# Performance work log

Hardware: AMD Instinct MI355X
Metric: run time of the kernel (lower is better)

## Reference

```python
import jax, jax.numpy as jnp
import numpy as np

NUM_STEPS = 3
NUM_HEADS = 8
HEAD_DIM = 128
EPS = 1e-5


def layernorm(x, g, b):
    mu = jnp.mean(x, -1, keepdims=True)
    var = jnp.mean(jnp.square(x - mu), -1, keepdims=True)
    return (x - mu) * jax.lax.rsqrt(var + EPS) * g + b


def entmax15(x):
    # Exact entmax-1.5 along last axis (Peters & Martins 2019, sort-based).
    x = (x - jnp.max(x, -1, keepdims=True)) / 2.0
    xs = jnp.flip(jnp.sort(x, -1), -1)  # descending sort
    rho = jnp.arange(1, x.shape[-1] + 1, dtype=x.dtype)
    mean = jnp.cumsum(xs, -1) / rho
    meansq = jnp.cumsum(xs * xs, -1) / rho
    ss = rho * (meansq - jnp.square(mean))
    tau = mean - jnp.sqrt(jnp.clip((1.0 - ss) / rho, 0.0, None))
    support = jnp.sum(tau <= xs, -1, keepdims=True)
    tau_star = jnp.take_along_axis(tau, support - 1, -1)
    return jnp.square(jnp.clip(x - tau_star, 0.0, None))


def setup_inputs() -> dict:
    key = jax.random.key(0)
    ks = jax.random.split(key, 6)
    B, S, Hd, Md, N = 2, 1024, 2048, 1024, 2048
    THD = NUM_HEADS * HEAD_DIM
    return {
        "hidden": jax.random.normal(ks[0], (B, S, Hd), jnp.float32),
        "memory": jax.random.normal(ks[1], (N, Md), jnp.float32),
        "Wq": jax.random.normal(ks[2], (THD, Hd), jnp.float32) / np.float32(np.sqrt(Hd)),
        "Wk": jax.random.normal(ks[3], (THD, Md), jnp.float32) / np.float32(np.sqrt(Md)),
        "Wv": jax.random.normal(ks[4], (THD, Md), jnp.float32) / np.float32(np.sqrt(Md)),
        "Wo": jax.random.normal(ks[5], (Hd, THD), jnp.float32) / np.float32(np.sqrt(THD)),
        "log_beta": jnp.full((NUM_HEADS,), float(np.log(1.0 / np.sqrt(HEAD_DIM))), jnp.float32),
        "g_state": jnp.ones((Hd,), jnp.float32),
        "b_state": jnp.zeros((Hd,), jnp.float32),
        "g_mem": jnp.ones((Md,), jnp.float32),
        "b_mem": jnp.zeros((Md,), jnp.float32),
    }


def reference(hidden, memory, Wq, Wk, Wv, Wo, log_beta, g_state, b_state, g_mem, b_mem):
    B, S, _ = hidden.shape
    N = memory.shape[0]
    H, hd = NUM_HEADS, HEAD_DIM
    # projections
    Q = layernorm(hidden, g_state, b_state) @ Wq.T            # (B,S,H*hd)
    mn = layernorm(memory, g_mem, b_mem)                      # (N,Md)
    K = (mn @ Wk.T).reshape(N, H, hd).transpose(1, 0, 2)      # (H,N,hd)
    V = (mn @ Wv.T).reshape(N, H, hd).transpose(1, 0, 2)      # (H,N,hd)
    xi = Q.reshape(B, S, H, hd).transpose(0, 2, 1, 3)          # (B,H,S,hd)
    beta = jnp.exp(log_beta)[None, :, None, None]
    for _ in range(NUM_STEPS):
        scores = jnp.einsum('bhsd,hnd->bhsn', xi, K) * beta    # (B,H,S,N)
        w = entmax15(scores)
        xi = jnp.einsum('bhsn,hnd->bhsd', w, V)
    out = xi.transpose(0, 2, 1, 3).reshape(B, S, H * hd) @ Wo.T  # (B,S,hidden_dim)
    return out
```

## Files before the change

kernel.cpp:

```cpp
#include <hip/hip_runtime.h>

typedef _Float16 half8 __attribute__((ext_vector_type(8)));
typedef _Float16 hv4 __attribute__((ext_vector_type(4)));
typedef float fv4 __attribute__((ext_vector_type(4)));

typedef __attribute__((address_space(3))) unsigned lds_u32;
typedef const __attribute__((address_space(1))) unsigned glb_u32;

__device__ __forceinline__ void gll16(const void* g, void* l) {
  __builtin_amdgcn_global_load_lds((glb_u32*)g, (lds_u32*)l, 16, 0, 0);
}

__global__ __launch_bounds__(256) void ln_rows(const float* __restrict__ in,
                                               const float* __restrict__ g,
                                               const float* __restrict__ bb,
                                               _Float16* __restrict__ out, int ncols) {
  __shared__ float sm[8];
  int row = blockIdx.x, t = threadIdx.x;
  const float* rp = in + (size_t)row * ncols;
  int nv = ncols >> 10;
  fv4 v[2];
  float s1 = 0.f, s2 = 0.f;
#pragma unroll
  for (int c = 0; c < 2; ++c)
    if (c < nv) {
      v[c] = *(const fv4*)(rp + c * 1024 + t * 4);
#pragma unroll
      for (int j = 0; j < 4; ++j) { s1 += v[c][j]; s2 += v[c][j] * v[c][j]; }
    }
#pragma unroll
  for (int off = 32; off > 0; off >>= 1) { s1 += __shfl_xor(s1, off, 64); s2 += __shfl_xor(s2, off, 64); }
  int w = t >> 6;
  if ((t & 63) == 0) { sm[w] = s1; sm[4 + w] = s2; }
  __syncthreads();
  s1 = sm[0] + sm[1] + sm[2] + sm[3];
  s2 = sm[4] + sm[5] + sm[6] + sm[7];
  float inv = 1.0f / (float)ncols;
  float mu = s1 * inv;
  float var = s2 * inv - mu * mu;
  float rstd = rsqrtf(var + 1e-5f);
#pragma unroll
  for (int c = 0; c < 2; ++c)
    if (c < nv) {
      int col = c * 1024 + t * 4;
      fv4 gg = *(const fv4*)(g + col);
      fv4 bv = *(const fv4*)(bb + col);
      hv4 o;
#pragma unroll
      for (int j = 0; j < 4; ++j) o[j] = (_Float16)(((v[c][j] - mu) * rstd) * gg[j] + bv[j]);
      *(hv4*)(out + (size_t)row * ncols + col) = o;
    }
}

__global__ __launch_bounds__(256) void cast_f16(const float* __restrict__ in,
                                                _Float16* __restrict__ out, int n) {
  int i = (blockIdx.x * 256 + threadIdx.x) << 2;
  if (i < n) {
    fv4 f = *(const fv4*)(in + i);
    hv4 h;
#pragma unroll
    for (int j = 0; j < 4; ++j) h[j] = (_Float16)f[j];
    *(hv4*)(out + i) = h;
  }
}

__global__ __launch_bounds__(256) void reduce_split(const float* __restrict__ parts, int ns,
                                                    long long stride,
                                                    _Float16* __restrict__ hi, int n) {
  int i = (blockIdx.x * 256 + threadIdx.x) << 2;
  if (i < n) {
    fv4 s = *(const fv4*)(parts + i);
    for (int j = 1; j < ns; ++j) {
      fv4 v = *(const fv4*)(parts + (size_t)j * stride + i);
      s += v;
    }
    hv4 h;
#pragma unroll
    for (int j = 0; j < 4; ++j) h[j] = (_Float16)s[j];
    *(hv4*)(hi + i) = h;
  }
}

__global__ __launch_bounds__(256) void entmax_w(const _Float16* __restrict__ scores,
                                                _Float16* __restrict__ wout) {
  __shared__ float comp[4][512];
  int wid = threadIdx.x >> 6;
  int row = blockIdx.x * 4 + wid;
  int l = threadIdx.x & 63;
  unsigned long long lmask = (1ull << l) - 1ull;
  const half8* sp = (const half8*)(scores + (size_t)row * 2048);
  half8 hx[4];
#pragma unroll
  for (int i = 0; i < 4; ++i) hx[i] = sp[i * 64 + l];
  fv4 x[8], xx[8];
#pragma unroll
  for (int i = 0; i < 4; ++i)
#pragma unroll
    for (int j = 0; j < 8; ++j) x[i * 2 + (j >> 2)][j & 3] = (float)hx[i][j];
  float m = x[0][0];
#pragma unroll
  for (int i = 0; i < 8; ++i)
#pragma unroll
    for (int j = 0; j < 4; ++j) m = fmaxf(m, x[i][j]);
#pragma unroll
  for (int off = 32; off > 0; off >>= 1) m = fmaxf(m, __shfl_xor(m, off, 64));
#pragma unroll
  for (int i = 0; i < 8; ++i)
#pragma unroll
    for (int j = 0; j < 4; ++j) {
      x[i][j] = (x[i][j] - m) * 0.5f;
      xx[i][j] = x[i][j] * x[i][j];
    }

  float tau = -1.0f;
  bool fixed = false;
  int cnti = 2048;
  for (int it = 0; it < 6 && !fixed; ++it) {
    float s1 = 0.f, s2 = 0.f;
    cnti = 0;
#pragma unroll
    for (int i = 0; i < 8; ++i)
#pragma unroll
      for (int j = 0; j < 4; ++j) {
        bool a = x[i][j] > tau;
        cnti += (int)__builtin_popcountll(__ballot(a));
        s1 += a ? x[i][j] : 0.f;
        s2 += a ? xx[i][j] : 0.f;
      }
#pragma unroll
    for (int off = 32; off > 0; off >>= 1) {
      s1 += __shfl_xor(s1, off, 64);
      s2 += __shfl_xor(s2, off, 64);
    }
    float cnt = (float)cnti;
    float mean = s1 / cnt;
    float ss = s2 - s1 * mean;
    float nt = mean - sqrtf(fmaxf((1.0f - ss) / cnt, 0.0f));
    if (nt == tau) fixed = true;
    else tau = nt;
    if (cnti <= 512) break;
  }
  if (!fixed) {
    if (cnti <= 512) {
      int base = 0;
#pragma unroll
      for (int i = 0; i < 8; ++i)
#pragma unroll
        for (int j = 0; j < 4; ++j) {
          bool a = x[i][j] > tau;
          unsigned long long mk = __ballot(a);
          if (a) comp[wid][base + (int)__builtin_popcountll(mk & lmask)] = x[i][j];
          base += (int)__builtin_popcountll(mk);
        }
      float y[8], yy[8];
#pragma unroll
      for (int r = 0; r < 8; ++r) {
        int idx = r * 64 + l;
        float v = (idx < base) ? comp[wid][idx] : -2.0f;
        y[r] = v;
        yy[r] = v * v;
      }
      for (int it = 0; it < 10 && !fixed; ++it) {
        float s1 = 0.f, s2 = 0.f;
        int c = 0;
#pragma unroll
        for (int r = 0; r < 8; ++r) {
          bool a = y[r] > tau;
          c += (int)__builtin_popcountll(__ballot(a));
          s1 += a ? y[r] : 0.f;
          s2 += a ? yy[r] : 0.f;
        }
#pragma unroll
        for (int off = 32; off > 0; off >>= 1) {
          s1 += __shfl_xor(s1, off, 64);
          s2 += __shfl_xor(s2, off, 64);
        }
        float cnt = (float)c;
        float mean = s1 / cnt;
        float ss = s2 - s1 * mean;
        float nt = mean - sqrtf(fmaxf((1.0f - ss) / cnt, 0.0f));
        if (nt == tau) fixed = true;
        else tau = nt;
      }
    } else {
      for (int it = 0; it < 8 && !fixed; ++it) {
        float s1 = 0.f, s2 = 0.f;
        int c = 0;
#pragma unroll
        for (int i = 0; i < 8; ++i)
#pragma unroll
          for (int j = 0; j < 4; ++j) {
            bool a = x[i][j] > tau;
            c += (int)__builtin_popcountll(__ballot(a));
            s1 += a ? x[i][j] : 0.f;
            s2 += a ? xx[i][j] : 0.f;
          }
#pragma unroll
        for (int off = 32; off > 0; off >>= 1) {
          s1 += __shfl_xor(s1, off, 64);
          s2 += __shfl_xor(s2, off, 64);
        }
        float cnt = (float)c;
        float mean = s1 / cnt;
        float ss = s2 - s1 * mean;
        float nt = mean - sqrtf(fmaxf((1.0f - ss) / cnt, 0.0f));
        if (nt == tau) fixed = true;
        else tau = nt;
      }
    }
  }

  half8* wp = (half8*)(wout + (size_t)row * 2048);
#pragma unroll
  for (int i = 0; i < 4; ++i) {
    half8 o;
#pragma unroll
    for (int j = 0; j < 8; ++j) {
      float d = fmaxf(x[i * 2 + (j >> 2)][j & 3] - tau, 0.f);
      o[j] = (_Float16)(d * d);
    }
    wp[i * 64 + l] = o;
  }
}

struct GemmParams {
  const _Float16 *A, *B, *B2;
  _Float16 *C16, *C16b;
  float* C32;
  const float* log_beta;
  int K, lda, ldb;
  long long aSB, aSH, bSH;
  long long cSB, cSH, cOsR, cOsC;
  long long cOsRb, cOsCb;
  long long partStride;
  int alphaMode, outMode, outModeB, nsplit, dual;
};

__global__ __launch_bounds__(256) void gemm_nt(GemmParams p) {
  __shared__ __align__(16) _Float16 As[128 * 32];
  __shared__ __align__(16) _Float16 Bs[128 * 32];
  int t = threadIdx.x;
  int m0 = blockIdx.y * 128;
  int bx = blockIdx.x, n0, kbeg, kend, ks = 0;
  if (p.nsplit > 1) {
    ks = bx % p.nsplit;
    n0 = (bx / p.nsplit) * 128;
    int kl = p.K / p.nsplit;
    kbeg = ks * kl;
    kend = kbeg + kl;
  } else {
    n0 = bx * 128;
    kbeg = 0;
    kend = p.K;
  }
  int z = blockIdx.z, bidx, h, job = 0;
  if (p.dual) { job = z; bidx = 0; h = 0; }
  else { bidx = z >> 3; h = z & 7; }
  const _Float16* pA = p.A + bidx * p.aSB + h * p.aSH;
  const _Float16* pB = (job ? p.B2 : p.B) + h * p.bSH;

  fv4 acc[4][4] = {};
  int wv = t >> 6, l = t & 63, quad = l >> 4, lr = l & 15;
  int wm = (wv >> 1) * 64, wn = (wv & 1) * 64;
  int rl = l >> 2, cl = (l & 3) * 8;

  for (int k0 = kbeg; k0 < kend; k0 += 32) {
#pragma unroll
    for (int v = 0; v < 2; ++v) {
      int rb = wv * 16 + v * 64;
      size_t aOff = (size_t)(m0 + rb + rl) * p.lda + k0 + cl;
      size_t bOff = (size_t)(n0 + rb + rl) * p.ldb + k0 + cl;
      gll16(pA + aOff, &As[rb * 32]);
      gll16(pB + bOff, &Bs[rb * 32]);
    }
    __syncthreads();
    half8 ah[4], bh[4];
#pragma unroll
    for (int mi = 0; mi < 4; ++mi) ah[mi] = *(const half8*)&As[(wm + mi * 16 + lr) * 32 + quad * 8];
#pragma unroll
    for (int ni = 0; ni < 4; ++ni) bh[ni] = *(const half8*)&Bs[(wn + ni * 16 + lr) * 32 + quad * 8];
#pragma unroll
    for (int mi = 0; mi < 4; ++mi)
#pragma unroll
      for (int ni = 0; ni < 4; ++ni)
        acc[mi][ni] = __builtin_amdgcn_mfma_f32_16x16x32_f16(ah[mi], bh[ni], acc[mi][ni], 0, 0, 0);
    __syncthreads();
  }

  float alpha = p.alphaMode ? __expf(p.log_beta[h]) : 1.0f;
  int om = (p.dual && job) ? p.outModeB : p.outMode;
  _Float16* c16 = (p.dual && job) ? p.C16b : p.C16;
  long long osR = (p.dual && job) ? p.cOsRb : p.cOsR;
  long long osC = (p.dual && job) ? p.cOsCb : p.cOsC;
  float* c32 = p.C32 + (p.nsplit > 1 ? (long long)ks * p.partStride : 0);
  long long cOff = (long long)bidx * p.cSB + (long long)h * p.cSH;
#pragma unroll
  for (int mi = 0; mi < 4; ++mi)
#pragma unroll
    for (int ni = 0; ni < 4; ++ni) {
      int row = m0 + wm + mi * 16 + quad * 4;
      int col = n0 + wn + ni * 16 + lr;
#pragma unroll
      for (int r = 0; r < 4; ++r) {
        float val = acc[mi][ni][r] * alpha;
        long long idx = cOff + (long long)(row + r) * osR + (long long)col * osC;
        if (om == 1) c32[idx] = val;
        else c16[idx] = (_Float16)val;
      }
    }
}

extern "C" void kernel_launch(void* const* d_in, const int* in_sizes, int n_in,
                              void* d_out, int out_size, void* d_ws, size_t ws_size,
                              hipStream_t stream) {
  const float* hidden = (const float*)d_in[0];
  const float* memory = (const float*)d_in[1];
  const float* Wq = (const float*)d_in[2];
  const float* Wk = (const float*)d_in[3];
  const float* Wv = (const float*)d_in[4];
  const float* Wo = (const float*)d_in[5];
  const float* log_beta = (const float*)d_in[6];
  const float* g_state = (const float*)d_in[7];
  const float* b_state = (const float*)d_in[8];
  const float* g_mem = (const float*)d_in[9];
  const float* b_mem = (const float*)d_in[10];

  char* w = (char*)d_ws;
  auto alloc = [&](size_t bytes) {
    char* r = w;
    w += (bytes + 255) & ~(size_t)255;
    return r;
  };
  _Float16* wq16 = (_Float16*)alloc(2097152 * 2);
  _Float16* wk16 = (_Float16*)alloc(1048576 * 2);
  _Float16* wv16 = (_Float16*)alloc(1048576 * 2);
  _Float16* wo16 = (_Float16*)alloc(2097152 * 2);
  _Float16* lnh16 = (_Float16*)alloc(4194304 * 2);
  _Float16* mn16 = (_Float16*)alloc(2097152 * 2);
  _Float16* kph = (_Float16*)alloc(2097152 * 2);
  _Float16* vt16 = (_Float16*)alloc(2097152 * 2);
  _Float16* xih = (_Float16*)alloc(2097152 * 2);
  float* parts = (float*)alloc((size_t)8 * 2097152 * 4);
  _Float16* scores16 = (_Float16*)alloc((size_t)33554432 * 2);

  ln_rows<<<2048, 256, 0, stream>>>(hidden, g_state, b_state, lnh16, 2048);
  ln_rows<<<2048, 256, 0, stream>>>(memory, g_mem, b_mem, mn16, 1024);
  cast_f16<<<2048, 256, 0, stream>>>(Wq, wq16, 2097152);
  cast_f16<<<1024, 256, 0, stream>>>(Wk, wk16, 1048576);
  cast_f16<<<1024, 256, 0, stream>>>(Wv, wv16, 1048576);
  cast_f16<<<2048, 256, 0, stream>>>(Wo, wo16, 2097152);

  {
    GemmParams p{};
    p.A = lnh16; p.lda = 2048;
    p.B = wq16; p.ldb = 2048;
    p.K = 2048; p.nsplit = 2;
    p.C32 = parts; p.outMode = 1; p.partStride = 2097152;
    p.cOsR = 1024; p.cOsC = 1;
    gemm_nt<<<dim3(16, 16, 1), 256, 0, stream>>>(p);
    reduce_split<<<2048, 256, 0, stream>>>(parts, 2, 2097152, xih, 2097152);
  }
  {
    GemmParams p{};
    p.A = mn16; p.lda = 1024;
    p.B = wk16; p.B2 = wv16; p.ldb = 1024;
    p.K = 1024; p.dual = 1;
    p.C16 = kph; p.outMode = 0; p.cOsR = 1024; p.cOsC = 1;
    p.C16b = vt16; p.outModeB = 0; p.cOsRb = 1; p.cOsCb = 2048;
    gemm_nt<<<dim3(8, 16, 2), 256, 0, stream>>>(p);
  }

  for (int step = 0; step < 3; ++step) {
    {
      GemmParams p{};
      p.A = xih;
      p.lda = 1024; p.aSB = 1048576; p.aSH = 128;
      p.B = kph; p.ldb = 1024; p.bSH = 128;
      p.K = 128;
      p.alphaMode = 1; p.log_beta = log_beta;
      p.C16 = scores16; p.outMode = 0;
      p.cSB = 16777216; p.cSH = 2097152;
      p.cOsR = 2048; p.cOsC = 1;
      gemm_nt<<<dim3(16, 8, 16), 256, 0, stream>>>(p);
    }
    entmax_w<<<4096, 256, 0, stream>>>(scores16, scores16);
    {
      GemmParams p{};
      p.A = scores16;
      p.lda = 2048; p.aSB = 16777216; p.aSH = 2097152;
      p.B = vt16; p.ldb = 2048; p.bSH = 262144;
      p.K = 2048; p.nsplit = 4;
      p.C32 = parts; p.outMode = 1; p.partStride = 2097152;
      p.cSB = 1048576; p.cSH = 128;
      p.cOsR = 1024; p.cOsC = 1;
      gemm_nt<<<dim3(4, 8, 16), 256, 0, stream>>>(p);
    }
    reduce_split<<<2048, 256, 0, stream>>>(parts, 4, 2097152, xih, 2097152);
  }

  {
    GemmParams p{};
    p.A = xih; p.lda = 1024;
    p.B = wo16; p.ldb = 1024;
    p.K = 1024;
    p.C32 = (float*)d_out; p.outMode = 1;
    p.cOsR = 2048; p.cOsC = 1;
    gemm_nt<<<dim3(16, 16, 1), 256, 0, stream>>>(p);
  }
}
```

Baseline: 493.7 us.

## Fuse entmax weight computation into the PV GEMM A-tile load via per-row threshold

The entmax kernel now writes only a per-row threshold (0.5*max + tau) and no longer writes the full fp16 weight matrix. The PV GEMM gains a template mode that loads raw scores through registers and computes max(0.5*s - c, 0)^2 in fp16 before storing into a padded LDS tile. This removes the write of the 2048-wide weight matrix per row, at the cost of losing the async global-to-LDS load for A and doing the elementwise work and its fp16 rounding inside the GEMM. The x*x temporaries in the entmax iterations are also replaced with FMAs to cut register use.

```diff
diff --git a/kernel.cpp b/kernel.cpp
--- a/kernel.cpp
+++ b/kernel.cpp
@@ -81,8 +81,8 @@
   }
 }
 
-__global__ __launch_bounds__(256) void entmax_w(const _Float16* __restrict__ scores,
-                                                _Float16* __restrict__ wout) {
+__global__ __launch_bounds__(256) void entmax_c(const _Float16* __restrict__ scores,
+                                                float* __restrict__ crow) {
   __shared__ float comp[4][512];
   int wid = threadIdx.x >> 6;
   int row = blockIdx.x * 4 + wid;
@@ -92,7 +92,7 @@
   half8 hx[4];
 #pragma unroll
   for (int i = 0; i < 4; ++i) hx[i] = sp[i * 64 + l];
-  fv4 x[8], xx[8];
+  fv4 x[8];
 #pragma unroll
   for (int i = 0; i < 4; ++i)
 #pragma unroll
@@ -107,10 +107,7 @@
 #pragma unroll
   for (int i = 0; i < 8; ++i)
 #pragma unroll
-    for (int j = 0; j < 4; ++j) {
-      x[i][j] = (x[i][j] - m) * 0.5f;
-      xx[i][j] = x[i][j] * x[i][j];
-    }
+    for (int j = 0; j < 4; ++j) x[i][j] = (x[i][j] - m) * 0.5f;
 
   float tau = -1.0f;
   bool fixed = false;
@@ -124,8 +121,9 @@
       for (int j = 0; j < 4; ++j) {
         bool a = x[i][j] > tau;
         cnti += (int)__builtin_popcountll(__ballot(a));
-        s1 += a ? x[i][j] : 0.f;
-        s2 += a ? xx[i][j] : 0.f;
+        float sel = a ? x[i][j] : 0.f;
+        s1 += sel;
+        s2 = fmaf(sel, sel, s2);
       }
 #pragma unroll
     for (int off = 32; off > 0; off >>= 1) {
@@ -152,13 +150,11 @@
           if (a) comp[wid][base + (int)__builtin_popcountll(mk & lmask)] = x[i][j];
           base += (int)__builtin_popcountll(mk);
         }
-      float y[8], yy[8];
+      float y[8];
 #pragma unroll
       for (int r = 0; r < 8; ++r) {
         int idx = r * 64 + l;
-        float v = (idx < base) ? comp[wid][idx] : -2.0f;
-        y[r] = v;
-        yy[r] = v * v;
+        y[r] = (idx < base) ? comp[wid][idx] : -2.0f;
       }
       for (int it = 0; it < 10 && !fixed; ++it) {
         float s1 = 0.f, s2 = 0.f;
@@ -167,8 +163,9 @@
         for (int r = 0; r < 8; ++r) {
           bool a = y[r] > tau;
           c += (int)__builtin_popcountll(__ballot(a));
-          s1 += a ? y[r] : 0.f;
-          s2 += a ? yy[r] : 0.f;
+          float sel = a ? y[r] : 0.f;
+          s1 += sel;
+          s2 = fmaf(sel, sel, s2);
         }
 #pragma unroll
         for (int off = 32; off > 0; off >>= 1) {
@@ -192,8 +189,9 @@
           for (int j = 0; j < 4; ++j) {
             bool a = x[i][j] > tau;
             c += (int)__builtin_popcountll(__ballot(a));
-            s1 += a ? x[i][j] : 0.f;
-            s2 += a ? xx[i][j] : 0.f;
+            float sel = a ? x[i][j] : 0.f;
+            s1 += sel;
+            s2 = fmaf(sel, sel, s2);
           }
 #pragma unroll
         for (int off = 32; off > 0; off >>= 1) {
@@ -210,34 +208,28 @@
     }
   }
 
-  half8* wp = (half8*)(wout + (size_t)row * 2048);
-#pragma unroll
-  for (int i = 0; i < 4; ++i) {
-    half8 o;
-#pragma unroll
-    for (int j = 0; j < 8; ++j) {
-      float d = fmaxf(x[i * 2 + (j >> 2)][j & 3] - tau, 0.f);
-      o[j] = (_Float16)(d * d);
-    }
-    wp[i * 64 + l] = o;
-  }
+  if (l == 0) crow[row] = 0.5f * m + tau;
 }
 
 struct GemmParams {
   const _Float16 *A, *B, *B2;
+  const float* crow;
   _Float16 *C16, *C16b;
   float* C32;
   const float* log_beta;
   int K, lda, ldb;
   long long aSB, aSH, bSH;
+  long long crowSB, crowSH;
   long long cSB, cSH, cOsR, cOsC;
   long long cOsRb, cOsCb;
   long long partStride;
   int alphaMode, outMode, outModeB, nsplit, dual;
 };
 
+template <int AMODE>
 __global__ __launch_bounds__(256) void gemm_nt(GemmParams p) {
-  __shared__ __align__(16) _Float16 As[128 * 32];
+  constexpr int AST = AMODE ? 40 : 32;
+  __shared__ __align__(16) _Float16 As[128 * AST];
   __shared__ __align__(16) _Float16 Bs[128 * 32];
   int t = threadIdx.x;
   int m0 = blockIdx.y * 128;
@@ -258,6 +250,7 @@
   else { bidx = z >> 3; h = z & 7; }
   const _Float16* pA = p.A + bidx * p.aSB + h * p.aSH;
   const _Float16* pB = (job ? p.B2 : p.B) + h * p.bSH;
+  const float* pc = AMODE ? p.crow + bidx * p.crowSB + h * p.crowSH : nullptr;
 
   fv4 acc[4][4] = {};
   int wv = t >> 6, l = t & 63, quad = l >> 4, lr = l & 15;
@@ -268,15 +261,25 @@
 #pragma unroll
     for (int v = 0; v < 2; ++v) {
       int rb = wv * 16 + v * 64;
-      size_t aOff = (size_t)(m0 + rb + rl) * p.lda + k0 + cl;
-      size_t bOff = (size_t)(n0 + rb + rl) * p.ldb + k0 + cl;
-      gll16(pA + aOff, &As[rb * 32]);
+      int r = rb + rl;
+      size_t aOff = (size_t)(m0 + r) * p.lda + k0 + cl;
+      size_t bOff = (size_t)(n0 + r) * p.ldb + k0 + cl;
+      if (AMODE == 0) {
+        gll16(pA + aOff, &As[rb * 32]);
+      } else {
+        half8 s8 = *(const half8*)(pA + aOff);
+        _Float16 c0 = (_Float16)pc[m0 + r];
+        half8 d = s8 * (_Float16)0.5f - c0;
+        d = __builtin_elementwise_max(d, (half8)(0));
+        half8 w8 = d * d;
+        *(half8*)&As[r * AST + cl] = w8;
+      }
       gll16(pB + bOff, &Bs[rb * 32]);
     }
     __syncthreads();
     half8 ah[4], bh[4];
 #pragma unroll
-    for (int mi = 0; mi < 4; ++mi) ah[mi] = *(const half8*)&As[(wm + mi * 16 + lr) * 32 + quad * 8];
+    for (int mi = 0; mi < 4; ++mi) ah[mi] = *(const half8*)&As[(wm + mi * 16 + lr) * AST + quad * 8];
 #pragma unroll
     for (int ni = 0; ni < 4; ++ni) bh[ni] = *(const half8*)&Bs[(wn + ni * 16 + lr) * 32 + quad * 8];
 #pragma unroll
@@ -342,6 +345,7 @@
   _Float16* xih = (_Float16*)alloc(2097152 * 2);
   float* parts = (float*)alloc((size_t)8 * 2097152 * 4);
   _Float16* scores16 = (_Float16*)alloc((size_t)33554432 * 2);
+  float* crow = (float*)alloc(16384 * 4);
 
   ln_rows<<<2048, 256, 0, stream>>>(hidden, g_state, b_state, lnh16, 2048);
   ln_rows<<<2048, 256, 0, stream>>>(memory, g_mem, b_mem, mn16, 1024);
@@ -357,7 +361,7 @@
     p.K = 2048; p.nsplit = 2;
     p.C32 = parts; p.outMode = 1; p.partStride = 2097152;
     p.cOsR = 1024; p.cOsC = 1;
-    gemm_nt<<<dim3(16, 16, 1), 256, 0, stream>>>(p);
+    gemm_nt<0><<<dim3(16, 16, 1), 256, 0, stream>>>(p);
     reduce_split<<<2048, 256, 0, stream>>>(parts, 2, 2097152, xih, 2097152);
   }
   {
@@ -367,7 +371,7 @@
     p.K = 1024; p.dual = 1;
     p.C16 = kph; p.outMode = 0; p.cOsR = 1024; p.cOsC = 1;
     p.C16b = vt16; p.outModeB = 0; p.cOsRb = 1; p.cOsCb = 2048;
-    gemm_nt<<<dim3(8, 16, 2), 256, 0, stream>>>(p);
+    gemm_nt<0><<<dim3(8, 16, 2), 256, 0, stream>>>(p);
   }
 
   for (int step = 0; step < 3; ++step) {
@@ -381,19 +385,20 @@
       p.C16 = scores16; p.outMode = 0;
       p.cSB = 16777216; p.cSH = 2097152;
       p.cOsR = 2048; p.cOsC = 1;
-      gemm_nt<<<dim3(16, 8, 16), 256, 0, stream>>>(p);
-    }
-    entmax_w<<<4096, 256, 0, stream>>>(scores16, scores16);
+      gemm_nt<0><<<dim3(16, 8, 16), 256, 0, stream>>>(p);
+    }
+    entmax_c<<<4096, 256, 0, stream>>>(scores16, crow);
     {
       GemmParams p{};
-      p.A = scores16;
+      p.A = scores16; p.crow = crow;
       p.lda = 2048; p.aSB = 16777216; p.aSH = 2097152;
+      p.crowSB = 8192; p.crowSH = 1024;
       p.B = vt16; p.ldb = 2048; p.bSH = 262144;
       p.K = 2048; p.nsplit = 4;
       p.C32 = parts; p.outMode = 1; p.partStride = 2097152;
       p.cSB = 1048576; p.cSH = 128;
       p.cOsR = 1024; p.cOsC = 1;
-      gemm_nt<<<dim3(4, 8, 16), 256, 0, stream>>>(p);
+      gemm_nt<1><<<dim3(4, 8, 16), 256, 0, stream>>>(p);
     }
     reduce_split<<<2048, 256, 0, stream>>>(parts, 4, 2097152, xih, 2097152);
   }
@@ -405,6 +410,6 @@
     p.K = 1024;
     p.C32 = (float*)d_out; p.outMode = 1;
     p.cOsR = 2048; p.cOsC = 1;
-    gemm_nt<<<dim3(16, 16, 1), 256, 0, stream>>>(p);
-  }
-}
+    gemm_nt<0><<<dim3(16, 16, 1), 256, 0, stream>>>(p);
+  }
+}
```

Result: faster. 478.8 us (-3.0%).
